# Kernel optimization log

Measured on AMD Instinct MI355X. Metric: run time of the kernel, lower is better.

The kernel has to match this reference:

```python
import jax, jax.numpy as jnp
import numpy as np

TEMPERATURE = 0.1


def setup_inputs() -> dict:
    key = jax.random.key(0)
    k1, k2 = jax.random.split(key)
    N, D = 8192, 128
    feature_embeds = jax.random.normal(k1, (N, D), dtype=jnp.float32)
    label_ids = jax.random.randint(k2, (N,), 0, 33, dtype=jnp.int64)
    return {"feature_embeds": feature_embeds, "label_ids": label_ids}


def reference(feature_embeds, label_ids):
    # L2-normalize embeddings (original applies F.normalize twice; idempotent)
    x = feature_embeds / jnp.linalg.norm(feature_embeds, axis=-1, keepdims=True)

    N = x.shape[0]
    # pairwise similarity logits [N, N]
    logits = (x @ x.T) / TEMPERATURE

    same = (label_ids[:, None] == label_ids[None, :]).astype(x.dtype)
    eye = jnp.eye(N, dtype=x.dtype)
    numerator_mask = same * (1.0 - eye)      # positives, excluding self
    denominator_mask = 1.0 - eye             # all others, excluding self

    e = jnp.exp(logits)
    Z = jnp.sum(e * denominator_mask, axis=-1)           # [N]
    # log(exp(logits)/Z) = logits - log Z
    log_prob = logits - jnp.log(Z)[:, None]

    pos_count = jnp.sum(numerator_mask, axis=-1)         # [N]
    valid = pos_count > 0
    per_row = jnp.sum(log_prob * numerator_mask, axis=-1) / jnp.where(valid, pos_count, 1.0)
    per_row = jnp.where(valid, per_row, 0.0)
    n_valid = jnp.sum(valid.astype(x.dtype))
    loss = -jnp.sum(per_row) / n_valid
    return loss
```

## Files before the change

### kernel.cpp

```cpp
#include <hip/hip_runtime.h>
#include <math.h>

#define NN 8192
#define DD 128
#define JR 32
#define NT ((NN / JR) / 64)
#define SQKE 3.7982825f
#define LN2 0.6931471805599453f
#define NCLS 33

typedef __attribute__((ext_vector_type(8))) short short8;
typedef __attribute__((ext_vector_type(4))) float f32x4;

__device__ __forceinline__ unsigned short f2bf(float f) {
    unsigned u = __builtin_bit_cast(unsigned, f);
    unsigned r = (u + 0x7FFFu + ((u >> 16) & 1u)) >> 16;
    return (unsigned short)r;
}
__device__ __forceinline__ float bf2f(unsigned short h) {
    unsigned u = ((unsigned)h) << 16;
    return __builtin_bit_cast(float, u);
}

__global__ __launch_bounds__(256) void prep_kernel(const float* __restrict__ x,
                                                   unsigned short* __restrict__ xn,
                                                   float* __restrict__ sd,
                                                   float* __restrict__ zs) {
    const int b = blockIdx.x, t = threadIdx.x;
    const int zi = b * 256 + t;
    if (zi < 2 * NN + 64) zs[zi] = 0.f;

    int row  = (b << 2) + (t >> 6);
    int lane = t & 63;
    float2 v = ((const float2*)(x + (size_t)row * DD))[lane];
    float ss = v.x * v.x + v.y * v.y;
    #pragma unroll
    for (int off = 32; off; off >>= 1) ss += __shfl_xor(ss, off);
    float rs = rsqrtf(ss) * SQKE;
    unsigned short bx = f2bf(v.x * rs), by = f2bf(v.y * rs);
    ushort2 st; st.x = bx; st.y = by;
    ((ushort2*)(xn + (size_t)row * DD))[lane] = st;
    float fx = bf2f(bx), fy = bf2f(by);
    float s2 = fx * fx + fy * fy;
    #pragma unroll
    for (int off = 32; off; off >>= 1) s2 += __shfl_xor(s2, off);
    if (lane == 0) sd[row] = s2;
}

__global__ __launch_bounds__(512, 2) void cl_main(const unsigned short* __restrict__ xn,
                                                  const int* __restrict__ labels,
                                                  float* __restrict__ Z,
                                                  float* __restrict__ S) {
    __shared__ __align__(16) unsigned short Bt[2][64][DD];

    const int tid  = threadIdx.x;
    const int w    = tid >> 6;
    const int lane = tid & 63;
    const int l15  = lane & 15;
    const int lhi  = lane >> 4;
    const int b    = (int)blockIdx.x;
    const int jr   = b & (JR - 1);
    const int panel = b >> 5;
    const int row0  = panel * 512 + w * 64;
    const int j0r   = jr * (NN / JR);

    short8 a[4][4];
    #pragma unroll
    for (int mi = 0; mi < 4; ++mi)
        #pragma unroll
        for (int ks = 0; ks < 4; ++ks)
            a[mi][ks] = *(const short8*)(xn + (size_t)(row0 + mi * 16 + l15) * DD + ks * 32 + lhi * 8);

    int labI[4][4];
    #pragma unroll
    for (int mi = 0; mi < 4; ++mi)
        #pragma unroll
        for (int r = 0; r < 4; ++r)
            labI[mi][r] = labels[row0 + mi * 16 + lhi * 4 + r];

    const int r4 = lane >> 4, kk = lane & 15;
    const int srow0 = w * 8 + r4;
    const int srow1 = w * 8 + 4 + r4;
    const unsigned short* sg0 = xn + (size_t)(j0r + srow0) * DD + (kk ^ (srow0 & 7)) * 8;
    const unsigned short* sg1 = xn + (size_t)(j0r + srow1) * DD + (kk ^ (srow1 & 7)) * 8;

    float z[4][4], s[4][4];
    #pragma unroll
    for (int mi = 0; mi < 4; ++mi)
        #pragma unroll
        for (int r = 0; r < 4; ++r) { z[mi][r] = 0.f; s[mi][r] = 0.f; }

    {
        short8 t0 = *(const short8*)sg0;
        short8 t1 = *(const short8*)sg1;
        *(short8*)&Bt[0][srow0][kk * 8] = t0;
        *(short8*)&Bt[0][srow1][kk * 8] = t1;
    }
    __syncthreads();

    const int sw = l15 & 7;
    int cur = 0;
    for (int t8 = 0; t8 < NT; ++t8) {
        const int j0 = j0r + t8 * 64;

        short8 nx0, nx1;
        if (t8 < NT - 1) {
            nx0 = *(const short8*)(sg0 + (size_t)(t8 + 1) * 64 * DD);
            nx1 = *(const short8*)(sg1 + (size_t)(t8 + 1) * 64 * DD);
        }
        int lj[4];
        #pragma unroll
        for (int ni = 0; ni < 4; ++ni) lj[ni] = labels[j0 + ni * 16 + l15];

        const char* rbase = (const char*)&Bt[cur][0][0] + l15 * 256;
        f32x4 acc[4][4];
        #pragma unroll
        for (int mi = 0; mi < 4; ++mi)
            #pragma unroll
            for (int ni = 0; ni < 4; ++ni) acc[mi][ni] = (f32x4){0.f, 0.f, 0.f, 0.f};

        #pragma unroll
        for (int ni = 0; ni < 4; ++ni) {
            short8 bfv[4];
            #pragma unroll
            for (int ks = 0; ks < 4; ++ks)
                bfv[ks] = *(const short8*)(rbase + ni * 4096 + ((((ks << 2) | lhi) ^ sw) << 4));
            #pragma unroll
            for (int ks = 0; ks < 4; ++ks)
                #pragma unroll
                for (int mi = 0; mi < 4; ++mi)
                    acc[mi][ni] = __builtin_amdgcn_mfma_f32_16x16x32_bf16(a[mi][ks], bfv[ks], acc[mi][ni], 0, 0, 0);
        }

        #pragma unroll
        for (int mi = 0; mi < 4; ++mi)
            #pragma unroll
            for (int ni = 0; ni < 4; ++ni)
                #pragma unroll
                for (int r = 0; r < 4; ++r) {
                    float d = acc[mi][ni][r];
                    z[mi][r] += __builtin_amdgcn_exp2f(d);
                    s[mi][r] += (lj[ni] == labI[mi][r]) ? d : 0.f;
                }

        if (t8 < NT - 1) {
            *(short8*)&Bt[cur ^ 1][srow0][kk * 8] = nx0;
            *(short8*)&Bt[cur ^ 1][srow1][kk * 8] = nx1;
        }
        __syncthreads();
        cur ^= 1;
    }

    #pragma unroll
    for (int mi = 0; mi < 4; ++mi)
        #pragma unroll
        for (int r = 0; r < 4; ++r) {
            float zz = z[mi][r], ss = s[mi][r];
            #pragma unroll
            for (int off = 1; off < 16; off <<= 1) {
                zz += __shfl_xor(zz, off);
                ss += __shfl_xor(ss, off);
            }
            if (l15 == 0) {
                int row = row0 + mi * 16 + lhi * 4 + r;
                atomicAdd(&Z[row], zz);
                atomicAdd(&S[row], ss);
            }
        }
}

__global__ __launch_bounds__(256) void fin1(const float* __restrict__ Z,
                                            const float* __restrict__ S,
                                            const float* __restrict__ sd,
                                            const int* __restrict__ labels,
                                            float* __restrict__ psum,
                                            float* __restrict__ pcnt) {
    __shared__ int cnt[NCLS];
    __shared__ float rs[4], rc[4];
    const int t = threadIdx.x;
    if (t < NCLS) cnt[t] = 0;
    __syncthreads();
    for (int i = t; i < NN; i += 256) atomicAdd(&cnt[labels[i]], 1);
    __syncthreads();

    const int row = blockIdx.x * 256 + t;
    float Zr = Z[row] - __builtin_amdgcn_exp2f(sd[row]);
    float Sr = S[row] - sd[row];
    int C = cnt[labels[row]] - 1;
    float pr = 0.f, vl = 0.f;
    if (C > 0) { pr = LN2 * Sr / (float)C - logf(Zr); vl = 1.f; }
    #pragma unroll
    for (int off = 32; off; off >>= 1) { pr += __shfl_xor(pr, off); vl += __shfl_xor(vl, off); }
    int wv = t >> 6, ln = t & 63;
    if (ln == 0) { rs[wv] = pr; rc[wv] = vl; }
    __syncthreads();
    if (t == 0) {
        psum[blockIdx.x] = rs[0] + rs[1] + rs[2] + rs[3];
        pcnt[blockIdx.x] = rc[0] + rc[1] + rc[2] + rc[3];
    }
}

__global__ void fin2(const float* __restrict__ psum, const float* __restrict__ pcnt,
                     float* __restrict__ out) {
    int t = threadIdx.x;
    float a = t < 32 ? psum[t] : 0.f;
    float c = t < 32 ? pcnt[t] : 0.f;
    #pragma unroll
    for (int off = 32; off; off >>= 1) { a += __shfl_xor(a, off); c += __shfl_xor(c, off); }
    if (t == 0) out[0] = -a / c;
}

extern "C" void kernel_launch(void* const* d_in, const int* in_sizes, int n_in,
                              void* d_out, int out_size, void* d_ws, size_t ws_size,
                              hipStream_t stream) {
    const float* x      = (const float*)d_in[0];
    const int*   labels = (const int*)d_in[1];
    float* out = (float*)d_out;
    char*  ws  = (char*)d_ws;

    size_t off = 0;
    unsigned short* xn = (unsigned short*)(ws + off); off += (size_t)NN * DD * 2;
    float* sd = (float*)(ws + off); off += (size_t)NN * 4;
    float* zs = (float*)(ws + off); off += (size_t)(2 * NN + 64) * 4;
    float* Z    = zs;
    float* S    = zs + NN;
    float* psum = zs + 2 * NN;
    float* pcnt = zs + 2 * NN + 32;

    prep_kernel<<<NN / 4, 256, 0, stream>>>(x, xn, sd, zs);
    cl_main<<<(NN / 512) * JR, 512, 0, stream>>>(xn, labels, Z, S);
    fin1<<<NN / 256, 256, 0, stream>>>(Z, S, sd, labels, psum, pcnt);
    fin2<<<1, 64, 0, stream>>>(psum, pcnt, out);
}
```

Baseline: 104.2 us.

## Exploit symmetry of similarity matrix by computing only upper-triangular tiles

Blocks now cover only the upper-triangular set of 256x256 tiles, indexed by a triangular mapping from the block id. Each off-diagonal tile adds its row sums and also its column sums to Z and S, using the symmetry of x·xᵀ. This roughly halves the MFMA and exp work. In exchange it adds extra register accumulators, more atomics, and smaller 256-thread blocks.

```diff
diff --git a/kernel.cpp b/kernel.cpp
--- a/kernel.cpp
+++ b/kernel.cpp
@@ -3,8 +3,9 @@
 
 #define NN 8192
 #define DD 128
-#define JR 32
-#define NT ((NN / JR) / 64)
+#define NPAN 32
+#define NT 4
+#define NBLK (NPAN * (NPAN + 1) / 2)
 #define SQKE 3.7982825f
 #define LN2 0.6931471805599453f
 #define NCLS 33
@@ -21,6 +22,7 @@
     unsigned u = ((unsigned)h) << 16;
     return __builtin_bit_cast(float, u);
 }
+__device__ __forceinline__ int offp(int p) { return 32 * p - (p * (p - 1)) / 2; }
 
 __global__ __launch_bounds__(256) void prep_kernel(const float* __restrict__ x,
                                                    unsigned short* __restrict__ xn,
@@ -47,10 +49,10 @@
     if (lane == 0) sd[row] = s2;
 }
 
-__global__ __launch_bounds__(512, 2) void cl_main(const unsigned short* __restrict__ xn,
-                                                  const int* __restrict__ labels,
-                                                  float* __restrict__ Z,
-                                                  float* __restrict__ S) {
+__global__ __launch_bounds__(256) void cl_main(const unsigned short* __restrict__ xn,
+                                               const int* __restrict__ labels,
+                                               float* __restrict__ Z,
+                                               float* __restrict__ S) {
     __shared__ __align__(16) unsigned short Bt[2][64][DD];
 
     const int tid  = threadIdx.x;
@@ -58,11 +60,16 @@
     const int lane = tid & 63;
     const int l15  = lane & 15;
     const int lhi  = lane >> 4;
-    const int b    = (int)blockIdx.x;
-    const int jr   = b & (JR - 1);
-    const int panel = b >> 5;
-    const int row0  = panel * 512 + w * 64;
-    const int j0r   = jr * (NN / JR);
+
+    const int e = (int)blockIdx.x;
+    int p = (int)((65.0f - sqrtf(4225.0f - 8.0f * (float)e)) * 0.5f);
+    while (p > 0 && offp(p) > e) --p;
+    while (offp(p + 1) <= e) ++p;
+    const int q = p + (e - offp(p));
+    const bool emitCol = (q > p);
+
+    const int row0  = p * 256 + w * 64;
+    const int jbase = q * 256;
 
     short8 a[4][4];
     #pragma unroll
@@ -78,35 +85,40 @@
         for (int r = 0; r < 4; ++r)
             labI[mi][r] = labels[row0 + mi * 16 + lhi * 4 + r];
 
-    const int r4 = lane >> 4, kk = lane & 15;
-    const int srow0 = w * 8 + r4;
-    const int srow1 = w * 8 + 4 + r4;
-    const unsigned short* sg0 = xn + (size_t)(j0r + srow0) * DD + (kk ^ (srow0 & 7)) * 8;
-    const unsigned short* sg1 = xn + (size_t)(j0r + srow1) * DD + (kk ^ (srow1 & 7)) * 8;
+    const int srow = tid >> 2, c4 = tid & 3;
+    const unsigned short* sgr = xn + (size_t)(jbase + srow) * DD;
 
     float z[4][4], s[4][4];
     #pragma unroll
     for (int mi = 0; mi < 4; ++mi)
         #pragma unroll
         for (int r = 0; r < 4; ++r) { z[mi][r] = 0.f; s[mi][r] = 0.f; }
-
-    {
-        short8 t0 = *(const short8*)sg0;
-        short8 t1 = *(const short8*)sg1;
-        *(short8*)&Bt[0][srow0][kk * 8] = t0;
-        *(short8*)&Bt[0][srow1][kk * 8] = t1;
+    float zc[NT][4], sc[NT][4];
+    #pragma unroll
+    for (int t8 = 0; t8 < NT; ++t8)
+        #pragma unroll
+        for (int ni = 0; ni < 4; ++ni) { zc[t8][ni] = 0.f; sc[t8][ni] = 0.f; }
+
+    #pragma unroll
+    for (int k = 0; k < 4; ++k) {
+        int blk = c4 + 4 * k;
+        short8 v = *(const short8*)(sgr + (size_t)(blk ^ (srow & 7)) * 8);
+        *(short8*)&Bt[0][srow][blk * 8] = v;
     }
     __syncthreads();
 
     const int sw = l15 & 7;
-    int cur = 0;
+    #pragma unroll
     for (int t8 = 0; t8 < NT; ++t8) {
-        const int j0 = j0r + t8 * 64;
-
-        short8 nx0, nx1;
+        const int cur = t8 & 1;
+        const int j0 = jbase + t8 * 64;
+
+        short8 nx[4];
         if (t8 < NT - 1) {
-            nx0 = *(const short8*)(sg0 + (size_t)(t8 + 1) * 64 * DD);
-            nx1 = *(const short8*)(sg1 + (size_t)(t8 + 1) * 64 * DD);
+            const unsigned short* sgn = sgr + (size_t)(t8 + 1) * 64 * DD;
+            #pragma unroll
+            for (int k = 0; k < 4; ++k)
+                nx[k] = *(const short8*)(sgn + (size_t)((c4 + 4 * k) ^ (srow & 7)) * 8);
         }
         int lj[4];
         #pragma unroll
@@ -139,16 +151,20 @@
                 #pragma unroll
                 for (int r = 0; r < 4; ++r) {
                     float d = acc[mi][ni][r];
-                    z[mi][r] += __builtin_amdgcn_exp2f(d);
-                    s[mi][r] += (lj[ni] == labI[mi][r]) ? d : 0.f;
+                    float ex = __builtin_amdgcn_exp2f(d);
+                    bool m = (lj[ni] == labI[mi][r]);
+                    z[mi][r] += ex;
+                    s[mi][r] += m ? d : 0.f;
+                    zc[t8][ni] += ex;
+                    sc[t8][ni] += m ? d : 0.f;
                 }
 
         if (t8 < NT - 1) {
-            *(short8*)&Bt[cur ^ 1][srow0][kk * 8] = nx0;
-            *(short8*)&Bt[cur ^ 1][srow1][kk * 8] = nx1;
+            #pragma unroll
+            for (int k = 0; k < 4; ++k)
+                *(short8*)&Bt[cur ^ 1][srow][(c4 + 4 * k) * 8] = nx[k];
         }
         __syncthreads();
-        cur ^= 1;
     }
 
     #pragma unroll
@@ -167,6 +183,22 @@
                 atomicAdd(&S[row], ss);
             }
         }
+
+    if (emitCol) {
+        #pragma unroll
+        for (int t8 = 0; t8 < NT; ++t8)
+            #pragma unroll
+            for (int ni = 0; ni < 4; ++ni) {
+                float zz = zc[t8][ni], ss = sc[t8][ni];
+                zz += __shfl_xor(zz, 16); zz += __shfl_xor(zz, 32);
+                ss += __shfl_xor(ss, 16); ss += __shfl_xor(ss, 32);
+                if (lhi == 0) {
+                    int col = jbase + t8 * 64 + ni * 16 + l15;
+                    atomicAdd(&Z[col], zz);
+                    atomicAdd(&S[col], ss);
+                }
+            }
+    }
 }
 
 __global__ __launch_bounds__(256) void fin1(const float* __restrict__ Z,
@@ -228,7 +260,7 @@
     float* pcnt = zs + 2 * NN + 32;
 
     prep_kernel<<<NN / 4, 256, 0, stream>>>(x, xn, sd, zs);
-    cl_main<<<(NN / 512) * JR, 512, 0, stream>>>(xn, labels, Z, S);
+    cl_main<<<NBLK, 256, 0, stream>>>(xn, labels, Z, S);
     fin1<<<NN / 256, 256, 0, stream>>>(Z, S, sd, labels, psum, pcnt);
     fin2<<<1, 64, 0, stream>>>(psum, pcnt, out);
 }
```

Measured after the change: 137.4 us. +31.8%, slower.
